# Performance work log

Measured on AMD Instinct MI355X. Metric: run time of the kernel, lower is better.

Reference implementation:

```python
import jax, jax.numpy as jnp
import numpy as np


def setup_inputs() -> dict:
    key = jax.random.key(0)
    k1, k2, k3 = jax.random.split(key, 3)
    bs, nvars, T, input_dim = 8, 16, 512, 256
    embed_dim, num_embed, codebook_num = 128, 512, 4
    inp = jax.random.normal(k1, (bs, nvars, T, input_dim), dtype=jnp.float32)
    # xavier_normal_ for (input_dim, embed_dim): std = sqrt(2/(fan_in+fan_out))
    xavier_std = float(np.sqrt(2.0 / (input_dim + embed_dim)))
    projector = jax.random.normal(k2, (input_dim, embed_dim), dtype=jnp.float32) * xavier_std
    codebook = jax.random.normal(k3, (codebook_num, num_embed, embed_dim), dtype=jnp.float32)
    return {"input": inp, "projector": projector, "codebook": codebook}


def reference(input, projector, codebook):
    # project: [b,n,t,input_dim] @ [input_dim,embed_dim] -> [b,n,t,d]
    x = jnp.matmul(input, projector)
    # L2-normalize along last dim (matches torch .norm(dim=-1,keepdim=True) division)
    x = x / jnp.linalg.norm(x, axis=-1, keepdims=True)
    cb = codebook / jnp.linalg.norm(codebook, axis=-1, keepdims=True)
    # cosine similarity: [b,n,t,c,m]
    similarity = jnp.einsum('bntd,cmd->bntcm', x, cb)
    # nearest code per codebook: [b,n,t,c]
    idx = jnp.argmax(similarity, axis=-1)
    return idx
```

## Files before the change

kernel.cpp:

```cpp
#include <hip/hip_runtime.h>
#include <math.h>

#define DIN    256
#define DEMB   128
#define NCB    4
#define MCODES 512
#define NCODE  2048
#define MARGIN 1.5e-4f

using bf16x8 = __attribute__((ext_vector_type(8))) short;
using f32x16 = __attribute__((ext_vector_type(16))) float;

static __device__ __forceinline__ unsigned short f2bf(float f) {
    unsigned u = __float_as_uint(f);
    u += 0x7FFFu + ((u >> 16) & 1u);
    return (unsigned short)(u >> 16);
}
static __device__ __forceinline__ float bf2f(unsigned short h) {
    return __uint_as_float(((unsigned)h) << 16);
}
static __device__ __forceinline__ float4 ld4(const float* p) {
    return *reinterpret_cast<const float4*>(p);
}
static __device__ __forceinline__ void gload_lds16(const void* g, void* l) {
    __builtin_amdgcn_global_load_lds(
        (const __attribute__((address_space(1))) void*)g,
        (__attribute__((address_space(3))) void*)l, 16, 0, 0);
}

__global__ __launch_bounds__(256) void prep_codebook(
        const float* __restrict__ cb, float* __restrict__ cbn,
        unsigned short* __restrict__ cbA) {
    const int w = threadIdx.x >> 6, lane = threadIdx.x & 63;
    const int code = blockIdx.x * 4 + w;
    const float2 v = reinterpret_cast<const float2*>(cb + (size_t)code * DEMB)[lane];
    float ss = v.x * v.x + v.y * v.y;
#pragma unroll
    for (int m = 1; m < 64; m <<= 1) ss += __shfl_xor(ss, m, 64);
    const float rn = 1.0f / sqrtf(ss);
    const float x0 = v.x * rn, x1 = v.y * rn;
    reinterpret_cast<float2*>(cbn + (size_t)code * DEMB)[lane] = make_float2(x0, x1);

    const unsigned short h0 = f2bf(x0), h1 = f2bf(x1);
    const unsigned short l0 = f2bf(x0 - bf2f(h0)), l1 = f2bf(x1 - bf2f(h1));
    const int ct = code >> 5, ci = code & 31;
    const int kt = lane >> 3, g = (lane >> 2) & 1, i = 2 * (lane & 3);
    const size_t base = ((size_t)ct * 1024 + kt * 128 + g * 32 + ci) * 8 + i;
    *reinterpret_cast<ushort2*>(cbA + base)       = make_ushort2(h0, h1);
    *reinterpret_cast<ushort2*>(cbA + base + 512) = make_ushort2(l0, l1);
}

__global__ __launch_bounds__(256) void prep_proj(
        const float* __restrict__ proj, unsigned short* __restrict__ pjA) {
    const int t = blockIdx.x * 256 + threadIdx.x;
    const int ci = t & 31, g = (t >> 5) & 1, kt = (t >> 6) & 15, mt = t >> 10;
    const int m = mt * 32 + ci;
    const size_t base = ((size_t)(mt * 16 + kt) * 3) * 512 + (size_t)(g * 32 + ci) * 8;
#pragma unroll
    for (int i = 0; i < 8; ++i) {
        const float v = proj[(size_t)(kt * 16 + g * 8 + i) * DEMB + m];
        const unsigned short h = f2bf(v);
        const float r1 = v - bf2f(h);
        const unsigned short md = f2bf(r1);
        const float r2 = r1 - bf2f(md);
        pjA[base + i]        = h;
        pjA[base + 512 + i]  = md;
        pjA[base + 1024 + i] = f2bf(r2);
    }
}

__global__ __launch_bounds__(256) void project_mfma(
        const float* __restrict__ inp, const unsigned short* __restrict__ pjA,
        float* __restrict__ xw) {
    const int tid = threadIdx.x;
    const int lane = tid & 63, mt = tid >> 6, kg = lane >> 5;
    const int row = blockIdx.x * 32 + (lane & 31);
    const float* xr = inp + (size_t)row * DIN;
    const unsigned short* pL = pjA + (size_t)lane * 8;

    auto ldin = [&](float4& a, float4& b, int kt) {
        a = ld4(xr + kt * 16 + kg * 8);
        b = ld4(xr + kt * 16 + kg * 8 + 4);
    };
    auto ldA = [&](bf16x8& h, bf16x8& m, bf16x8& l, int kt) {
        const unsigned short* pf = pL + ((size_t)(mt * 16 + kt) * 3) * 512;
        h = *reinterpret_cast<const bf16x8*>(pf);
        m = *reinterpret_cast<const bf16x8*>(pf + 512);
        l = *reinterpret_cast<const bf16x8*>(pf + 1024);
    };

    f32x16 P, Q;
#pragma unroll
    for (int r = 0; r < 16; ++r) { P[r] = 0.0f; Q[r] = 0.0f; }

    auto do_step = [&](const float4& c0, const float4& c1,
                       const bf16x8& Ah, const bf16x8& Am, const bf16x8& Al) {
        const float xs[8] = {c0.x, c0.y, c0.z, c0.w, c1.x, c1.y, c1.z, c1.w};
        bf16x8 Bh, Bm, Bl;
#pragma unroll
        for (int e = 0; e < 8; ++e) {
            const float v = xs[e];
            const unsigned short h = f2bf(v);
            const float r1 = v - bf2f(h);
            const unsigned short md = f2bf(r1);
            const float r2 = r1 - bf2f(md);
            Bh[e] = (short)h; Bm[e] = (short)md; Bl[e] = (short)f2bf(r2);
        }
        P = __builtin_amdgcn_mfma_f32_32x32x16_bf16(Ah, Bh, P, 0, 0, 0);
        Q = __builtin_amdgcn_mfma_f32_32x32x16_bf16(Ah, Bm, Q, 0, 0, 0);
        Q = __builtin_amdgcn_mfma_f32_32x32x16_bf16(Am, Bh, Q, 0, 0, 0);
        Q = __builtin_amdgcn_mfma_f32_32x32x16_bf16(Ah, Bl, Q, 0, 0, 0);
        Q = __builtin_amdgcn_mfma_f32_32x32x16_bf16(Al, Bh, Q, 0, 0, 0);
        Q = __builtin_amdgcn_mfma_f32_32x32x16_bf16(Am, Bm, Q, 0, 0, 0);
    };

    float4 iA0, iA1, iB0, iB1;
    bf16x8 hA, mA, lA, hB, mB, lB;
    ldin(iA0, iA1, 0); ldA(hA, mA, lA, 0);
    ldin(iB0, iB1, 1); ldA(hB, mB, lB, 1);

#pragma unroll 1
    for (int kt = 0; kt < 16; kt += 2) {
        do_step(iA0, iA1, hA, mA, lA);
        if (kt + 2 < 16) { ldin(iA0, iA1, kt + 2); ldA(hA, mA, lA, kt + 2); }
        do_step(iB0, iB1, hB, mB, lB);
        if (kt + 3 < 16) { ldin(iB0, iB1, kt + 3); ldA(hB, mB, lB, kt + 3); }
    }

#pragma unroll
    for (int q = 0; q < 4; ++q) {
        float4 v;
        v.x = P[q * 4 + 0] + Q[q * 4 + 0];
        v.y = P[q * 4 + 1] + Q[q * 4 + 1];
        v.z = P[q * 4 + 2] + Q[q * 4 + 2];
        v.w = P[q * 4 + 3] + Q[q * 4 + 3];
        *reinterpret_cast<float4*>(xw + (size_t)row * DEMB + mt * 32 + q * 8 + kg * 4) = v;
    }
}

__global__ __launch_bounds__(256) void project_kernel(
        const float* __restrict__ inp, const float* __restrict__ proj,
        float* __restrict__ xw) {
    const int tid = threadIdx.x, tx = tid & 31, ty = tid >> 5;
    const int rowBase = blockIdx.x * 64;

    float acc1[8][4];
#pragma unroll
    for (int i = 0; i < 8; ++i)
#pragma unroll
        for (int j = 0; j < 4; ++j) acc1[i][j] = 0.0f;

    const float* inRow0 = inp + (size_t)(rowBase + ty) * DIN;
    const float* pjCol  = proj + tx * 4;

    float4 ivA[8], ivB[8], pjA[4], pjB[4];
    auto load_step = [&](float4 iv[8], float4 pj[4], int kk) {
#pragma unroll
        for (int j = 0; j < 4; ++j) pj[j] = ld4(pjCol + (size_t)(kk + j) * DEMB);
#pragma unroll
        for (int i = 0; i < 8; ++i) iv[i] = ld4(inRow0 + (size_t)(8 * i) * DIN + kk);
    };
    auto fma_step = [&](const float4 iv[8], const float4 pj[4]) {
#pragma unroll
        for (int i = 0; i < 8; ++i) {
            const float* ivp = reinterpret_cast<const float*>(&iv[i]);
#pragma unroll
            for (int j = 0; j < 4; ++j) {
                acc1[i][0] = fmaf(ivp[j], pj[j].x, acc1[i][0]);
                acc1[i][1] = fmaf(ivp[j], pj[j].y, acc1[i][1]);
                acc1[i][2] = fmaf(ivp[j], pj[j].z, acc1[i][2]);
                acc1[i][3] = fmaf(ivp[j], pj[j].w, acc1[i][3]);
            }
        }
    };
    load_step(ivA, pjA, 0);
#pragma unroll 1
    for (int k = 0; k < DIN; k += 8) {
        load_step(ivB, pjB, k + 4);
        fma_step(ivA, pjA);
        if (k + 8 < DIN) load_step(ivA, pjA, k + 8);
        fma_step(ivB, pjB);
    }
#pragma unroll
    for (int i = 0; i < 8; ++i) {
        const int r = rowBase + ty + 8 * i;
        *reinterpret_cast<float4*>(xw + (size_t)r * DEMB + tx * 4) =
            make_float4(acc1[i][0], acc1[i][1], acc1[i][2], acc1[i][3]);
    }
}

__global__ __launch_bounds__(256) void sim_kernel(
        const float* __restrict__ xw,
        const unsigned short* __restrict__ cbA,
        int* __restrict__ out, int* __restrict__ unc_cnt,
        int* __restrict__ unc_list) {
    __shared__ __align__(16) short sA[3][8192];
    const int tid = threadIdx.x;
    const int lane = tid & 63, wv = tid >> 6;
    const int kg = lane >> 5;
    const int cbi = blockIdx.x & 3;
    const int rowBase = (blockIdx.x >> 2) * 128;
    const int row = rowBase + wv * 32 + (lane & 31);

    const short* gA = (const short*)cbA + (size_t)cbi * 16 * 8192;
    auto stage = [&](int buf, int t) {
        const short* g = gA + (size_t)t * 8192 + wv * 2048 + lane * 8;
        short* l = &sA[buf][wv * 2048];
#pragma unroll
        for (int c = 0; c < 4; ++c)
            gload_lds16(g + c * 512, l + c * 512);
    };

    stage(0, 0);
    stage(1, 1);

    bf16x8 Bhi[8], Blo[8];
    {
        const float* xr = xw + (size_t)row * DEMB;
        float4 f0[8], f1[8];
        float ss = 0.0f;
#pragma unroll
        for (int kt = 0; kt < 8; ++kt) {
            f0[kt] = ld4(xr + kt * 16 + kg * 8);
            f1[kt] = ld4(xr + kt * 16 + kg * 8 + 4);
            ss += f0[kt].x * f0[kt].x + f0[kt].y * f0[kt].y +
                  f0[kt].z * f0[kt].z + f0[kt].w * f0[kt].w +
                  f1[kt].x * f1[kt].x + f1[kt].y * f1[kt].y +
                  f1[kt].z * f1[kt].z + f1[kt].w * f1[kt].w;
        }
        ss += __shfl_xor(ss, 32, 64);
        const float rn = 1.0f / sqrtf(ss);
#pragma unroll
        for (int kt = 0; kt < 8; ++kt) {
            const float xs[8] = {f0[kt].x, f0[kt].y, f0[kt].z, f0[kt].w,
                                 f1[kt].x, f1[kt].y, f1[kt].z, f1[kt].w};
            bf16x8 hv, lv;
#pragma unroll
            for (int e = 0; e < 8; ++e) {
                const float xn = xs[e] * rn;
                const unsigned short h = f2bf(xn);
                hv[e] = (short)h;
                lv[e] = (short)f2bf(xn - bf2f(h));
            }
            Bhi[kt] = hv; Blo[kt] = lv;
        }
    }

    f32x16 TWO, ZERO;
#pragma unroll
    for (int r = 0; r < 16; ++r) { TWO[r] = 2.0f; ZERO[r] = 0.0f; }

    float t1 = -INFINITY, t2 = -INFINITY; int i1 = 0;
    f32x16 cA = TWO, cB1 = ZERO, cB2 = ZERO;

    auto epi = [&](const f32x16& vA, const f32x16& vB1, const f32x16& vB2,
                   int gprev) {
        const int base = gprev * 32;
#pragma unroll
        for (int r = 0; r < 16; ++r) {
            const float v = (vA[r] + vB1[r]) + vB2[r];
            const int gidx = base + (r & 3) + 8 * (r >> 2) + 4 * kg;
            t2 = fmaxf(t2, fminf(v, t1));
            if (v > t1) { t1 = v; i1 = gidx; }
        }
    };

#pragma unroll
    for (int g = 0; g < 16; ++g) {
        if (g < 15) asm volatile("s_waitcnt vmcnt(4)" ::: "memory");
        else        asm volatile("s_waitcnt vmcnt(0)" ::: "memory");
        __builtin_amdgcn_s_barrier();
        asm volatile("" ::: "memory");
        if (g + 2 < 16) stage((g + 2) % 3, g + 2);

        const short* pa = &sA[g % 3][lane * 8];
        f32x16 nA, nB1, nB2;
        __builtin_amdgcn_s_setprio(1);
#pragma unroll
        for (int kt = 0; kt < 8; ++kt) {
            const bf16x8 Ahi = *reinterpret_cast<const bf16x8*>(pa + kt * 1024);
            const bf16x8 Alo = *reinterpret_cast<const bf16x8*>(pa + kt * 1024 + 512);
            nA  = __builtin_amdgcn_mfma_f32_32x32x16_bf16(Ahi, Bhi[kt], kt ? nA  : TWO,  0, 0, 0);
            nB1 = __builtin_amdgcn_mfma_f32_32x32x16_bf16(Ahi, Blo[kt], kt ? nB1 : ZERO, 0, 0, 0);
            nB2 = __builtin_amdgcn_mfma_f32_32x32x16_bf16(Alo, Bhi[kt], kt ? nB2 : ZERO, 0, 0, 0);
        }
        __builtin_amdgcn_s_setprio(0);

        if (g > 0) epi(cA, cB1, cB2, g - 1);
        cA = nA; cB1 = nB1; cB2 = nB2;
    }
    epi(cA, cB1, cB2, 15);

    const float o1 = __shfl_xor(t1, 32, 64);
    const float o2 = __shfl_xor(t2, 32, 64);
    const int   oi = __shfl_xor(i1, 32, 64);
    const float m2 = fmaxf(fmaxf(t2, o2), fminf(t1, o1));
    if (o1 > t1 || (o1 == t1 && oi < i1)) { t1 = o1; i1 = oi; }
    const bool unc = (t1 - m2) < MARGIN;
    if (lane < 32 && !unc)
        out[(size_t)row * NCB + cbi] = i1;

    unsigned long long msk = __ballot(unc && lane < 32);
    if (lane == 0 && msk) {
        const int n = __popcll(msk);
        int base = atomicAdd(unc_cnt, n);
        while (msk) {
            const int r = __ffsll(msk) - 1; msk &= msk - 1;
            unc_list[base++] = ((rowBase + wv * 32 + r) << 2) | cbi;
        }
    }
}

__global__ __launch_bounds__(256) void recheck_kernel(
        const float* __restrict__ inp, const float* __restrict__ proj,
        const float* __restrict__ cbn,
        const int* __restrict__ unc_cnt, const int* __restrict__ unc_list,
        int* __restrict__ out) {
    __shared__ float sx[DEMB];
    __shared__ float sBest[4];
    __shared__ int   sIdx[4];
    const int lane = threadIdx.x & 63, wv = threadIdx.x >> 6;
    const int n = *unc_cnt;
    for (int it = blockIdx.x; it < n; it += gridDim.x) {
        const int item = unc_list[it];
        const int row = item >> 2, cbi = item & 3;
        if (wv == 0) {
            const float* ir = inp + (size_t)row * DIN;
            float a0 = 0.0f, a1 = 0.0f;
#pragma unroll 2
            for (int k = 0; k < DIN; k += 4) {
                const float4 iv = ld4(ir + k);
                const float* ivp = reinterpret_cast<const float*>(&iv);
#pragma unroll
                for (int j = 0; j < 4; ++j) {
                    a0 = fmaf(ivp[j], proj[(size_t)(k + j) * DEMB + lane],      a0);
                    a1 = fmaf(ivp[j], proj[(size_t)(k + j) * DEMB + lane + 64], a1);
                }
            }
            sx[lane] = a0; sx[lane + 64] = a1;
        }
        __syncthreads();

        float best = -INFINITY; int bi = 0;
#pragma unroll
        for (int j = 0; j < 2; ++j) {
            const int c = wv * 128 + lane + 64 * j;
            const float* cv = cbn + ((size_t)cbi * MCODES + c) * DEMB;
            float s0 = 0, s1 = 0, s2 = 0, s3 = 0;
#pragma unroll 4
            for (int k = 0; k < DEMB; k += 4) {
                const float4 xk = ld4(&sx[k]);
                const float4 ck = ld4(cv + k);
                s0 = fmaf(xk.x, ck.x, s0); s1 = fmaf(xk.y, ck.y, s1);
                s2 = fmaf(xk.z, ck.z, s2); s3 = fmaf(xk.w, ck.w, s3);
            }
            const float s = (s0 + s1) + (s2 + s3);
            if (s > best) { best = s; bi = c; }
        }
#pragma unroll
        for (int mm = 1; mm < 64; mm <<= 1) {
            const float ov = __shfl_xor(best, mm, 64);
            const int   oc = __shfl_xor(bi, mm, 64);
            if (ov > best || (ov == best && oc < bi)) { best = ov; bi = oc; }
        }
        if (lane == 0) { sBest[wv] = best; sIdx[wv] = bi; }
        __syncthreads();
        if (wv == 0 && lane == 0) {
            float b = sBest[0]; int bidx = sIdx[0];
#pragma unroll
            for (int w = 1; w < 4; ++w) {
                if (sBest[w] > b) { b = sBest[w]; bidx = sIdx[w]; }
            }
            out[(size_t)row * NCB + cbi] = bidx;
        }
        __syncthreads();
    }
}

__global__ __launch_bounds__(256) void fused_quantize_kernel(
        const float* __restrict__ inp, const float* __restrict__ proj,
        const float* __restrict__ cbn, const unsigned short* __restrict__ cbA,
        int* __restrict__ out) {
    __shared__ float sX[128][132];
    __shared__ float sRn[128];
    const int tid = threadIdx.x;
    const int tx = tid & 31, ty = tid >> 5;
    const int rowBase = blockIdx.x * 128;

#pragma unroll 1
    for (int p = 0; p < 2; ++p) {
        float acc1[8][4];
#pragma unroll
        for (int i = 0; i < 8; ++i)
#pragma unroll
            for (int j = 0; j < 4; ++j) acc1[i][j] = 0.0f;
        const float* inRow0 = inp + (size_t)(rowBase + p * 64 + ty) * DIN;
        const float* pjCol  = proj + tx * 4;
        float4 ivA[8], ivB[8], pjA[4], pjB[4];
        auto load_step = [&](float4 iv[8], float4 pj[4], int kk) {
#pragma unroll
            for (int j = 0; j < 4; ++j) pj[j] = ld4(pjCol + (size_t)(kk + j) * DEMB);
#pragma unroll
            for (int i = 0; i < 8; ++i) iv[i] = ld4(inRow0 + (size_t)(8 * i) * DIN + kk);
        };
        auto fma_step = [&](const float4 iv[8], const float4 pj[4]) {
#pragma unroll
            for (int i = 0; i < 8; ++i) {
                const float* ivp = reinterpret_cast<const float*>(&iv[i]);
#pragma unroll
                for (int j = 0; j < 4; ++j) {
                    acc1[i][0] = fmaf(ivp[j], pj[j].x, acc1[i][0]);
                    acc1[i][1] = fmaf(ivp[j], pj[j].y, acc1[i][1]);
                    acc1[i][2] = fmaf(ivp[j], pj[j].z, acc1[i][2]);
                    acc1[i][3] = fmaf(ivp[j], pj[j].w, acc1[i][3]);
                }
            }
        };
        load_step(ivA, pjA, 0);
#pragma unroll 1
        for (int k = 0; k < DIN; k += 8) {
            load_step(ivB, pjB, k + 4);
            fma_step(ivA, pjA);
            if (k + 8 < DIN) load_step(ivA, pjA, k + 8);
            fma_step(ivB, pjB);
        }
#pragma unroll
        for (int i = 0; i < 8; ++i) {
            const int r = p * 64 + ty + 8 * i;
            float ss = acc1[i][0] * acc1[i][0] + acc1[i][1] * acc1[i][1] +
                       acc1[i][2] * acc1[i][2] + acc1[i][3] * acc1[i][3];
#pragma unroll
            for (int mm = 1; mm < 32; mm <<= 1) ss += __shfl_xor(ss, mm, 64);
            if (tx == 0) sRn[r] = 1.0f / sqrtf(ss);
            *reinterpret_cast<float4*>(&sX[r][tx * 4]) =
                make_float4(acc1[i][0], acc1[i][1], acc1[i][2], acc1[i][3]);
        }
    }
    __syncthreads();

    const int lane = tid & 63, wv = tid >> 6;
    const int kg = lane >> 5;
    const int rowL = wv * 32 + (lane & 31);
    bf16x8 Bhi[8], Blo[8];
    {
        const float rn = sRn[rowL];
#pragma unroll
        for (int kt = 0; kt < 8; ++kt) {
            const int k0 = kt * 16 + kg * 8;
            float4 f0 = ld4(&sX[rowL][k0]);
            float4 f1 = ld4(&sX[rowL][k0 + 4]);
            float xs[8] = {f0.x, f0.y, f0.z, f0.w, f1.x, f1.y, f1.z, f1.w};
            bf16x8 hv, lv;
#pragma unroll
            for (int e = 0; e < 8; ++e) {
                const float xn = xs[e] * rn;
                const unsigned short h = f2bf(xn);
                hv[e] = (short)h;
                lv[e] = (short)f2bf(xn - bf2f(h));
            }
            Bhi[kt] = hv; Blo[kt] = lv;
        }
    }
    float t1 = -INFINITY, t2 = -INFINITY; int i1 = 0;
    const short* pA = reinterpret_cast<const short*>(cbA) + (size_t)lane * 8;
#pragma unroll 1
    for (int ct = 0; ct < 64; ++ct) {
        if ((ct & 1) == 0) __syncthreads();
        const short* pct = pA + (size_t)ct * 8192;
        f32x16 accA, accB;
#pragma unroll
        for (int r = 0; r < 16; ++r) { accA[r] = 0.0f; accB[r] = 0.0f; }
#pragma unroll
        for (int kt = 0; kt < 8; ++kt) {
            const bf16x8 Ahi = *reinterpret_cast<const bf16x8*>(pct + kt * 1024);
            const bf16x8 Alo = *reinterpret_cast<const bf16x8*>(pct + kt * 1024 + 512);
            accA = __builtin_amdgcn_mfma_f32_32x32x16_bf16(Ahi, Bhi[kt], accA, 0, 0, 0);
            accB = __builtin_amdgcn_mfma_f32_32x32x16_bf16(Ahi, Blo[kt], accB, 0, 0, 0);
            accB = __builtin_amdgcn_mfma_f32_32x32x16_bf16(Alo, Bhi[kt], accB, 0, 0, 0);
        }
#pragma unroll
        for (int r = 0; r < 16; ++r) {
            const float v = accA[r] + accB[r];
            const int gidx = ct * 32 + ((r & 3) + 8 * (r >> 2) + 4 * kg);
            t2 = fmaxf(t2, fminf(v, t1));
            if (v > t1) { t1 = v; i1 = gidx; }
        }
        if ((ct & 15) == 15) {
            const int cbi = ct >> 4;
            const float o1 = __shfl_xor(t1, 32, 64);
            const float o2 = __shfl_xor(t2, 32, 64);
            const int   oi = __shfl_xor(i1, 32, 64);
            const float m2 = fmaxf(fmaxf(t2, o2), fminf(t1, o1));
            if (o1 > t1 || (o1 == t1 && oi < i1)) { t1 = o1; i1 = oi; }
            const bool unc = (t1 - m2) < MARGIN;
            if (lane < 32 && !unc)
                out[(size_t)(rowBase + rowL) * NCB + cbi] = i1 - cbi * MCODES;
            unsigned long long msk = __ballot(unc && lane < 32);
            while (msk) {
                const int r = __ffsll(msk) - 1; msk &= msk - 1;
                const int rl = wv * 32 + r;
                float best = -INFINITY; int bi = 0;
#pragma unroll 1
                for (int j = 0; j < 8; ++j) {
                    const int c = lane + 64 * j;
                    const float* cv = cbn + ((size_t)cbi * MCODES + c) * DEMB;
                    float s0 = 0, s1 = 0, s2 = 0, s3 = 0;
#pragma unroll
                    for (int k = 0; k < DEMB; k += 4) {
                        const float4 xk = ld4(&sX[rl][k]);
                        const float4 ck = ld4(cv + k);
                        s0 = fmaf(xk.x, ck.x, s0); s1 = fmaf(xk.y, ck.y, s1);
                        s2 = fmaf(xk.z, ck.z, s2); s3 = fmaf(xk.w, ck.w, s3);
                    }
                    const float s = (s0 + s1) + (s2 + s3);
                    if (s > best) { best = s; bi = c; }
                }
#pragma unroll
                for (int mm = 1; mm < 64; mm <<= 1) {
                    const float ov = __shfl_xor(best, mm, 64);
                    const int   oc = __shfl_xor(bi, mm, 64);
                    if (ov > best || (ov == best && oc < bi)) { best = ov; bi = oc; }
                }
                if (lane == 0) out[(size_t)(rowBase + rl) * NCB + cbi] = bi;
            }
            t1 = -INFINITY; t2 = -INFINITY; i1 = 0;
        }
    }
}

extern "C" void kernel_launch(void* const* d_in, const int* in_sizes, int n_in,
                              void* d_out, int out_size, void* d_ws, size_t ws_size,
                              hipStream_t stream) {
    const float* inp  = (const float*)d_in[0];
    const float* proj = (const float*)d_in[1];
    const float* cb   = (const float*)d_in[2];
    int* out = (int*)d_out;

    char* ws = (char*)d_ws;
    float* cbn = (float*)ws;
    unsigned short* cbA = (unsigned short*)(ws + (1 << 20));
    float* xw  = (float*)(ws + (2 << 20) + (1 << 18));
    const size_t off_cnt = (size_t)(2 << 20) + (1 << 18) + ((size_t)32 << 20);
    int* unc_cnt  = (int*)(ws + off_cnt);
    int* unc_list = (int*)(ws + off_cnt + 256);
    const size_t off_pjA = off_cnt + 256 + (1 << 20);
    unsigned short* pjA = (unsigned short*)(ws + off_pjA);
    const size_t need_old = off_pjA;
    const size_t need_new = off_pjA + 192 * 1024;

    hipLaunchKernelGGL(prep_codebook, dim3(NCODE / 4), dim3(256), 0, stream,
                       cb, cbn, cbA);
    if (ws_size >= need_old) {
        hipMemsetAsync(unc_cnt, 0, 4, stream);
        if (ws_size >= need_new) {
            hipLaunchKernelGGL(prep_proj, dim3(16), dim3(256), 0, stream, proj, pjA);
            hipLaunchKernelGGL(project_mfma, dim3(2048), dim3(256), 0, stream,
                               inp, pjA, xw);
        } else {
            hipLaunchKernelGGL(project_kernel, dim3(1024), dim3(256), 0, stream,
                               inp, proj, xw);
        }
        hipLaunchKernelGGL(sim_kernel, dim3(2048), dim3(256), 0, stream,
                           xw, cbA, out, unc_cnt, unc_list);
        hipLaunchKernelGGL(recheck_kernel, dim3(2048), dim3(256), 0, stream,
                           inp, proj, cbn, unc_cnt, unc_list, out);
    } else {
        hipLaunchKernelGGL(fused_quantize_kernel, dim3(512), dim3(256), 0, stream,
                           inp, proj, cbn, cbA, out);
    }
}
```

Baseline: 219.6 us.

## Merge split-precision MFMA accumulators into one chain and stop unrolling group loop

The three separate accumulators for the hi·hi, hi·lo and lo·hi bf16 products are replaced by one accumulator chained through all MFMAs. This removes the per-element sum in the epilogue and frees accumulator registers. The group loop is no longer unrolled and the setprio hints are removed, which shrinks code size. The cost is a fully serial dependency chain across MFMAs, which can expose MFMA latency and reduce issue overlap.

```diff
diff --git a/kernel.cpp b/kernel.cpp
--- a/kernel.cpp
+++ b/kernel.cpp
@@ -246,26 +246,14 @@
         }
     }
 
-    f32x16 TWO, ZERO;
-#pragma unroll
-    for (int r = 0; r < 16; ++r) { TWO[r] = 2.0f; ZERO[r] = 0.0f; }
-
+    f32x16 TWO;
+#pragma unroll
+    for (int r = 0; r < 16; ++r) TWO[r] = 2.0f;
+
+    f32x16 acc = TWO;
     float t1 = -INFINITY, t2 = -INFINITY; int i1 = 0;
-    f32x16 cA = TWO, cB1 = ZERO, cB2 = ZERO;
-
-    auto epi = [&](const f32x16& vA, const f32x16& vB1, const f32x16& vB2,
-                   int gprev) {
-        const int base = gprev * 32;
-#pragma unroll
-        for (int r = 0; r < 16; ++r) {
-            const float v = (vA[r] + vB1[r]) + vB2[r];
-            const int gidx = base + (r & 3) + 8 * (r >> 2) + 4 * kg;
-            t2 = fmaxf(t2, fminf(v, t1));
-            if (v > t1) { t1 = v; i1 = gidx; }
-        }
-    };
-
-#pragma unroll
+
+#pragma unroll 1
     for (int g = 0; g < 16; ++g) {
         if (g < 15) asm volatile("s_waitcnt vmcnt(4)" ::: "memory");
         else        asm volatile("s_waitcnt vmcnt(0)" ::: "memory");
@@ -274,22 +262,37 @@
         if (g + 2 < 16) stage((g + 2) % 3, g + 2);
 
         const short* pa = &sA[g % 3][lane * 8];
-        f32x16 nA, nB1, nB2;
-        __builtin_amdgcn_s_setprio(1);
+        const f32x16 pAcc = acc;
 #pragma unroll
         for (int kt = 0; kt < 8; ++kt) {
             const bf16x8 Ahi = *reinterpret_cast<const bf16x8*>(pa + kt * 1024);
             const bf16x8 Alo = *reinterpret_cast<const bf16x8*>(pa + kt * 1024 + 512);
-            nA  = __builtin_amdgcn_mfma_f32_32x32x16_bf16(Ahi, Bhi[kt], kt ? nA  : TWO,  0, 0, 0);
-            nB1 = __builtin_amdgcn_mfma_f32_32x32x16_bf16(Ahi, Blo[kt], kt ? nB1 : ZERO, 0, 0, 0);
-            nB2 = __builtin_amdgcn_mfma_f32_32x32x16_bf16(Alo, Bhi[kt], kt ? nB2 : ZERO, 0, 0, 0);
-        }
-        __builtin_amdgcn_s_setprio(0);
-
-        if (g > 0) epi(cA, cB1, cB2, g - 1);
-        cA = nA; cB1 = nB1; cB2 = nB2;
-    }
-    epi(cA, cB1, cB2, 15);
+            acc = __builtin_amdgcn_mfma_f32_32x32x16_bf16(Ahi, Bhi[kt], kt ? acc : TWO, 0, 0, 0);
+            acc = __builtin_amdgcn_mfma_f32_32x32x16_bf16(Ahi, Blo[kt], acc, 0, 0, 0);
+            acc = __builtin_amdgcn_mfma_f32_32x32x16_bf16(Alo, Bhi[kt], acc, 0, 0, 0);
+        }
+
+        if (g > 0) {
+            const int base = (g - 1) * 32;
+#pragma unroll
+            for (int r = 0; r < 16; ++r) {
+                const float v = pAcc[r];
+                const int gidx = base + (r & 3) + 8 * (r >> 2) + 4 * kg;
+                t2 = fmaxf(t2, fminf(v, t1));
+                if (v > t1) { t1 = v; i1 = gidx; }
+            }
+        }
+    }
+    {
+        const int base = 15 * 32;
+#pragma unroll
+        for (int r = 0; r < 16; ++r) {
+            const float v = acc[r];
+            const int gidx = base + (r & 3) + 8 * (r >> 2) + 4 * kg;
+            t2 = fmaxf(t2, fminf(v, t1));
+            if (v > t1) { t1 = v; i1 = gidx; }
+        }
+    }
 
     const float o1 = __shfl_xor(t1, 32, 64);
     const float o2 = __shfl_xor(t2, 32, 64);
```

New measurement: 217.7 us. No clear change (-0.9%).
